# Kernel tuning notes

Hardware: AMD Instinct MI355X
Metric: run time of the kernel (lower is better)

## Reference

```python
import jax, jax.numpy as jnp
import numpy as np
from jax import lax

RATE = 2          # self.rate
KS = 3            # kernel_size for matching patches
FUSE_K = 3        # fuse_k
SCALE = 10.0      # softmax_scale
EPS = 1e-4        # NaN guard in l2 norm


def extract_patches(x, size=3, step=1):
    """ZeroPad2d(1) then unfold -> (B, L, C, size, size) with L = Ho*Wo."""
    B, C, H, W = x.shape
    p = lax.conv_general_dilated_patches(
        x, (size, size), (step, step), padding=((1, 1), (1, 1)))
    Ho, Wo = p.shape[2], p.shape[3]
    # feature dim ordering of patches is (C, kh, kw)
    p = p.reshape(B, C, size, size, Ho, Wo)
    return p.transpose(0, 4, 5, 1, 2, 3).reshape(B, Ho * Wo, C, size, size)


def fuse_conv(s):
    """Conv with identity eye(k) kernel, pad 1 (diagonal propagation)."""
    w = jnp.eye(FUSE_K, dtype=s.dtype).reshape(1, 1, FUSE_K, FUSE_K)
    return lax.conv_general_dilated(s, w, (1, 1), ((1, 1), (1, 1)))


def contextual_attention(foreground, background, mask):
    B, C, H, W = foreground.shape
    # raw patches used as deconv filters: (B, L, C, 2*rate, 2*rate)
    raw_w = extract_patches(background, size=2 * RATE, step=RATE)
    # nearest downsample by rate (F.interpolate nearest, scale 1/rate == stride slice)
    fg = foreground[:, :, ::RATE, ::RATE]
    bg = background[:, :, ::RATE, ::RATE]
    fh, fw = fg.shape[2], fg.shape[3]
    bh, bw = bg.shape[2], bg.shape[3]
    # matching patches: (B, L, C, 3, 3), L = bh*bw
    w = extract_patches(bg, KS, 1)
    # mask patches -> per-patch validity (code uses batch 0 of the mask only)
    m = mask[:, :, ::RATE, ::RATE]
    mp = extract_patches(m, KS, 1)[0]            # (L, 1, 3, 3)
    mm = jnp.mean(mp, axis=(1, 2, 3))            # (L,)
    eq = (mm == 0.0).astype(foreground.dtype)[None, :, None, None]  # (1, L, 1, 1)
    # cosine-normalized filters
    norm = jnp.sqrt(jnp.sum(w * w, axis=(2, 3, 4), keepdims=True))
    wn = w / jnp.maximum(norm, EPS)
    # per-batch dynamic conv: scores (B, L, fh, fw)
    def score(f, wi):
        return lax.conv_general_dilated(f[None], wi, (1, 1), ((1, 1), (1, 1)))[0]
    s = jax.vmap(score)(fg, wn)
    # fuse: two identity-kernel convs with raw reshapes (faithful to torch .view,
    # including the discarded second permute in the original code)
    s = s.reshape(B, 1, fh * fw, bh * bw)
    s = fuse_conv(s)
    s = s.reshape(B, fh, fw, bh, bw).transpose(0, 2, 1, 4, 3)
    s = s.reshape(B, 1, fh * fw, bh * bw)
    s = fuse_conv(s)
    s = s.reshape(B, bh * bw, fh, fw)  # raw row-major reinterpret, as torch .view does
    # masked scaled softmax over background-patch dim
    s = s * eq
    s = jax.nn.softmax(s * SCALE, axis=1) * eq
    # per-batch deconv with raw patches as filters (conv_transpose2d stride=rate, pad=1)
    def deconv(si, rwi):
        # torch conv_transpose2d(W:(L,C,4,4)) == dilated conv with flipped, swapped kernel
        wt = jnp.flip(rwi, axis=(-2, -1)).transpose(1, 0, 2, 3)  # (C, L, 4, 4)
        pad = 2 * RATE - 1 - 1  # k - 1 - padding = 2
        return lax.conv_general_dilated(
            si[None], wt, (1, 1), ((pad, pad), (pad, pad)),
            lhs_dilation=(RATE, RATE))[0]
    y = jax.vmap(deconv)(s, raw_w) / 4.0  # (B, C, H, W)
    return y


def setup_inputs() -> dict:
    key = jax.random.key(0)
    k1, k2, k3 = jax.random.split(key, 3)
    B, C, H, W = 8, 128, 64, 64
    foreground = jax.random.normal(k1, (B, C, H, W), jnp.float32)
    background = jax.random.normal(k2, (B, C, H, W), jnp.float32)
    mask = (jax.random.uniform(k3, (1, 1, H, W)) < 0.25).astype(jnp.float32)
    return {"foreground": foreground, "background": background, "mask": mask}


def reference(foreground, background, mask):
    return contextual_attention(foreground, background, mask)
```

## Files before the change

### kernel.cpp

```cpp
#include <hip/hip_runtime.h>

typedef _Float16 half8 __attribute__((ext_vector_type(8)));
typedef float f32x4 __attribute__((ext_vector_type(4)));
typedef unsigned short us8 __attribute__((ext_vector_type(8)));
typedef unsigned short ush;
typedef unsigned int uint32;

#define IMGB 295936u
#define WROW 8704u

#define OFF_FGH  0ull
#define OFF_BGH  2367488ull
#define OFF_BGL  4734976ull
#define OFF_BGT  7102464ull
#define OFF_SS   15523840ull
#define OFF_LIST 15589376ull
#define OFF_NACT 15593472ull
#define OFF_S0   15597568ull
#define OFF_S2   49152000ull
#define OFF_WGT2 82706432ull

static __device__ __forceinline__ ush f2h(float f) {
    union { _Float16 h; ush u; } c; c.h = (_Float16)f; return c.u;
}
static __device__ __forceinline__ float h2f(ush u) {
    union { _Float16 h; ush u; } c; c.u = u; return (float)c.h;
}
__device__ __forceinline__ int untr(int v) { return ((v & 31) << 5) | (v >> 5); }

__global__ void k_prep2(const float* __restrict__ fg, const float* __restrict__ bg,
                        const float* __restrict__ mask,
                        ush* __restrict__ fgh3, ush* __restrict__ bgh,
                        ush* __restrict__ bgl, ush* __restrict__ BGt,
                        float* __restrict__ SS, int* __restrict__ L,
                        int* __restrict__ nact) {
    int y = blockIdx.x, b = blockIdx.y, t = threadIdx.x;
    __shared__ float lds[64 * 129];
    __shared__ float fls[32 * 129];
    __shared__ float sm2[32][8];
    __shared__ int ps[256];
    if (y == 64) {
        if (b != 0) return;
        int fl[4], s = 0;
#pragma unroll
        for (int j = 0; j < 4; ++j) {
            int l = t * 4 + j;
            int hm = l >> 5, wm = l & 31;
            int any = 0;
            for (int di = -1; di <= 1; ++di)
                for (int dj = -1; dj <= 1; ++dj) {
                    int yy = hm + di, xxx = wm + dj;
                    if (yy >= 0 && yy < 32 && xxx >= 0 && xxx < 32)
                        any |= (mask[(2 * yy) * 64 + 2 * xxx] != 0.0f);
                }
            fl[j] = !any; s += fl[j];
        }
        ps[t] = s;
        __syncthreads();
        for (int off = 1; off < 256; off <<= 1) {
            int v = (t >= off) ? ps[t - off] : 0;
            __syncthreads();
            ps[t] += v;
            __syncthreads();
        }
        int base = ps[t] - s;
#pragma unroll
        for (int j = 0; j < 4; ++j)
            if (fl[j]) L[base++] = t * 4 + j;
        if (t == 255) nact[0] = ps[255];
        return;
    }
    int xx = t & 63;
    for (int c0 = 0; c0 < 128; c0 += 4) {
        int c = c0 + (t >> 6);
        lds[xx * 129 + c] = bg[((b * 128 + c) * 64 + y) * 64 + xx];
    }
    __syncthreads();
    uint32* dst = (uint32*)(BGt + (size_t)(b * 64 + y) * 8192);
    for (int j = t; j < 4096; j += 256) {
        int x = j >> 6, cp = (j & 63) * 2;
        uint32 h0 = f2h(lds[x * 129 + cp]);
        uint32 h1 = f2h(lds[x * 129 + cp + 1]);
        dst[j] = h0 | (h1 << 16);
    }
    if ((y & 1) != 0) return;
    int yd = y >> 1;
    {
        int xq = t & 31, cg = t >> 5;
        for (int c0 = 0; c0 < 128; c0 += 8) {
            int c = c0 + cg;
            fls[xq * 129 + c] = fg[((b * 128 + c) * 64 + y) * 64 + 2 * xq];
        }
    }
    {
        int xd = t & 31, part = t >> 5;
        float s = 0.f;
        int c0 = part * 16;
#pragma unroll
        for (int c = 0; c < 16; ++c) {
            float v = lds[(2 * xd) * 129 + c0 + c];
            s += v * v;
        }
        sm2[xd][part] = s;
    }
    __syncthreads();
    if (t < 32) {
        float s = 0.f;
#pragma unroll
        for (int p = 0; p < 8; ++p) s += sm2[t][p];
        SS[b * 1024 + yd * 32 + t] = s;
    }
    unsigned base = ((b * 34 + yd + 1) * 34 + 1) * 128;
    for (int k = t; k < 2048; k += 256) {
        int x = k >> 6, c = (k & 63) * 2;
        float vb0 = lds[(2 * x) * 129 + c], vb1 = lds[(2 * x) * 129 + c + 1];
        float vf0 = fls[x * 129 + c],       vf1 = fls[x * 129 + c + 1];
        _Float16 bh0 = (_Float16)vb0, bh1 = (_Float16)vb1;
        float br0 = vb0 - (float)bh0, br1 = vb1 - (float)bh1;
        union { _Float16 h; ush u; } x0, x1;
        x0.h = bh0; x1.h = bh1;
        uint32 b01 = (uint32)x0.u | ((uint32)x1.u << 16);
        uint32 l01 = (uint32)f2h(br0) | ((uint32)f2h(br1) << 16);
        ((uint32*)(bgh + base))[k] = b01;
        ((uint32*)(bgl + base))[k] = l01;
        uint32 f01 = (uint32)f2h(vf0) | ((uint32)f2h(vf1) << 16);
        int ch = c >> 6, g = (c >> 3) & 7, cl = c & 7;
        unsigned pix = (unsigned)(yd + 1) * 34 + (x + 1);
        unsigned ui = (((unsigned)(b * 16 + ch * 8 + g) * 1156 + pix) << 2) + (cl >> 1);
        ((uint32*)fgh3)[ui] = f01;
    }
    unsigned cb0 = ((unsigned)(b * 34 + yd + 1) * 34) * 64;
    if (t < 64) {
        ((uint32*)bgh)[cb0 + t] = 0; ((uint32*)bgl)[cb0 + t] = 0;
    } else if (t < 128) {
        unsigned cb1 = cb0 + 33 * 64 + (t - 64);
        ((uint32*)bgh)[cb1] = 0; ((uint32*)bgl)[cb1] = 0;
    } else if (t < 256) {
        int tt = t - 128;
        unsigned pix = (unsigned)(yd + 1) * 34 + ((tt >> 6) ? 33u : 0u);
        int pl = tt & 63, plane = pl >> 2, w = pl & 3;
        ((uint32*)fgh3)[(((unsigned)(b * 16 + plane) * 1156 + pix) << 2) + w] = 0;
    }
    if (yd == 0 || yd == 31) {
        int prow = (yd == 0) ? 0 : 33;
        unsigned rb = (unsigned)(b * 34 + prow) * 2176;
        for (int k = t; k < 2176; k += 256) {
            ((uint32*)bgh)[rb + k] = 0; ((uint32*)bgl)[rb + k] = 0;
            int plane = k / 136, rem = k - plane * 136;
            unsigned pix = (unsigned)prow * 34 + (rem >> 2);
            ((uint32*)fgh3)[(((unsigned)(b * 16 + plane) * 1156 + pix) << 2) + (rem & 3)] = 0;
        }
    }
}

__global__ __launch_bounds__(256, 2)
void k_smfma(const ush* __restrict__ fgh3, const ush* __restrict__ bgh,
             const ush* __restrict__ bgl, const float* __restrict__ SS,
             float* __restrict__ s0) {
    int qt = blockIdx.x, pt = blockIdx.y, b = blockIdx.z;
    int t = threadIdx.x, wid = t >> 6, lane = t & 63;
    int wp = wid >> 1, wq = wid & 1;
    __shared__ ulong2 smem_raw[3328];
    __shared__ float rnl[128];
    char* smem = (char*)smem_raw;

    if (t < 128) {
        int pr = (pt << 2) + (t >> 5), pc = t & 31;
        float n2 = 0.f;
#pragma unroll
        for (int di = -1; di <= 1; ++di) {
            int r = pr + di;
            if ((unsigned)r < 32u) {
                const float* Srow = SS + b * 1024 + r * 32;
#pragma unroll
                for (int dj = -1; dj <= 1; ++dj) {
                    int c2 = pc + dj;
                    if ((unsigned)c2 < 32u) n2 += Srow[c2];
                }
            }
        }
        rnl[t] = 1.0f / fmaxf(sqrtf(n2), 1e-4f);
    }

    const char* base0 = (const char*)bgh + (size_t)b * IMGB + (unsigned)(pt * 4) * WROW;
    const char* base1 = (const char*)bgl + (size_t)b * IMGB + (unsigned)(pt * 4) * WROW;

    f32x4 acc[4][4];
#pragma unroll
    for (int i = 0; i < 4; ++i)
#pragma unroll
        for (int j = 0; j < 4; ++j) acc[i][j] = (f32x4){0.f, 0.f, 0.f, 0.f};

    int r15 = lane & 15, hi2 = lane >> 4;
    for (int ch = 0; ch < 2; ++ch) {
        __syncthreads();
        {
            int pixl = (lane >> 3);
            int sl = lane & 7;
            for (int idx = wid; idx < 52; idx += 4) {
                int a = idx / 26;
                int chunk = idx - a * 26;
                int pix = chunk * 8 + pixl;
                int g = sl ^ (pix & 7);
                const char* sb = a ? base1 : base0;
                const char* gp = sb + ((unsigned)pix << 8) + ((unsigned)ch << 7)
                               + ((unsigned)g << 4);
                char* lp = smem + (unsigned)(a * 26624 + chunk * 1024);
                __builtin_amdgcn_global_load_lds(
                    (const __attribute__((address_space(1))) void*)gp,
                    (__attribute__((address_space(3))) void*)lp, 16, 0, 0);
            }
        }
        __syncthreads();

        const char* Aimg = (const char*)fgh3
                         + (((size_t)(b * 16 + ch * 8)) * 1156 + (unsigned)(qt * 136)) * 16;
        for (int o = 0; o < 9; ++o) {
            int dy = o / 3, dx = o - 3 * (o / 3);
            int pixB[4], pixA[4];
#pragma unroll
            for (int i = 0; i < 4; ++i) {
                pixB[i] = (wp * 2 + (i >> 1) + dy) * 34 + (i & 1) * 16 + r15 + dx;
                pixA[i] = (wq * 2 + (i >> 1) + dy) * 34 + (i & 1) * 16 + r15 + dx;
            }
#pragma unroll
            for (int cc = 0; cc < 2; ++cc) {
                int g = cc * 4 + hi2;
                half8 bh[4], bl[4], af[4];
#pragma unroll
                for (int i = 0; i < 4; ++i) {
                    unsigned offB = ((unsigned)pixB[i] << 7) + ((unsigned)(g ^ (pixB[i] & 7)) << 4);
                    bh[i] = *(const half8*)(smem + offB);
                    bl[i] = *(const half8*)(smem + 26624 + offB);
                    af[i] = *(const half8*)(Aimg + (((size_t)g * 1156 + pixA[i]) << 4));
                }
#pragma unroll
                for (int i = 0; i < 4; ++i)
#pragma unroll
                    for (int j = 0; j < 4; ++j) {
                        acc[i][j] = __builtin_amdgcn_mfma_f32_16x16x32_f16(bh[i], af[j], acc[i][j], 0, 0, 0);
                        acc[i][j] = __builtin_amdgcn_mfma_f32_16x16x32_f16(bl[i], af[j], acc[i][j], 0, 0, 0);
                    }
            }
        }
    }
    int col = lane & 15, rgrp = (lane >> 4) << 2;
#pragma unroll
    for (int i = 0; i < 4; ++i) {
        int Pl = wp * 64 + i * 16 + rgrp;
        int Pb = pt * 128 + Pl;
        float rn0 = rnl[Pl + 0];
        float rn1 = rnl[Pl + 1];
        float rn2 = rnl[Pl + 2];
        float rn3 = rnl[Pl + 3];
#pragma unroll
        for (int j = 0; j < 4; ++j) {
            int Q = qt * 128 + wq * 64 + j * 16 + col;
            float* dst = s0 + ((size_t)(b * 1024 + Pb) << 10) + Q;
            dst[0]    = acc[i][j][0] * rn0;
            dst[1024] = acc[i][j][1] * rn1;
            dst[2048] = acc[i][j][2] * rn2;
            dst[3072] = acc[i][j][3] * rn3;
        }
    }
}

__global__ void k_fuse(const float* __restrict__ s0, float* __restrict__ s2t,
                       const int* __restrict__ L, const int* __restrict__ nactp) {
    int nact = *nactp;
    int b = blockIdx.z;
    int u = blockIdx.x * 256 + threadIdx.x;
    int T = untr(u);
    const float* S = s0 + (size_t)b * 1048576;
    for (int ai = blockIdx.y; ai < nact; ai += 32) {
        int R = L[ai];
        float acc = 0.f;
#pragma unroll
        for (int k = -1; k <= 1; ++k) {
            int Rk = R + k, Tk = T + k;
            if ((unsigned)Rk < 1024u && (unsigned)Tk < 1024u) {
                int Pr = untr(Rk), Qc = untr(Tk);
#pragma unroll
                for (int j = -1; j <= 1; ++j) {
                    int r = Pr + j, cI = Qc + j;
                    if ((unsigned)r < 1024u && (unsigned)cI < 1024u)
                        acc += S[(size_t)r * 1024 + cI];
                }
            }
        }
        s2t[(size_t)b * 1048576 + (size_t)R * 1024 + u] = acc;
    }
}

__global__ __launch_bounds__(256)
void k_ctsw(const ush* __restrict__ BGt, const float* __restrict__ s2t,
            const int* __restrict__ L, const int* __restrict__ nactp,
            ush* __restrict__ CT, ush* __restrict__ W2) {
    int bx = blockIdx.x, b = blockIdx.y, t = threadIdx.x;
    int nact = *nactp;
    __shared__ float sm[32][8], sd[32][8];
    __shared__ float Msh[32], RDsh[32];
    __shared__ ush wt[32][136];
    if (bx < 16) {
        int KPAD = (nact + 31) & ~31;
        int ab = bx, a = ab >> 2, bb = ab & 3;
        for (int ai0 = 0; ai0 < KPAD; ai0 += 256) {
            int ai = ai0 + t;
            if (ai >= KPAD) break;
            int ok = 0;
            const ush* srow = nullptr;
            if (ai < nact) {
                int R = L[ai];
                int hb = R >> 5, wb = R & 31;
                int row = 2 * hb - 1 + a, col = 2 * wb - 1 + bb;
                if (row >= 0 && row < 64 && col >= 0 && col < 64) {
                    ok = 1;
                    srow = BGt + ((size_t)((b * 64 + row) * 64 + col) << 7);
                }
            }
            ush* dst = CT + ((size_t)(b * 16 + ab) << 15) + ai;
#pragma unroll 4
            for (int c = 0; c < 128; ++c)
                dst[(size_t)c << 8] = ok ? srow[c] : (ush)0;
        }
        return;
    }
    int uc = bx - 16;
    int u0 = uc * 32;
    int part = t >> 5, ul = t & 31;
    {
        const float* S = s2t + (size_t)b * 1048576 + u0 + ul;
        float m = -3e38f, d = 0.f;
        for (int ai = part; ai < nact; ai += 8) {
            float v = S[(size_t)L[ai] << 10];
            if (v > m) { d *= expf(10.f * (m - v)); m = v; }
            d += expf(10.f * (v - m));
        }
        sm[ul][part] = m; sd[ul][part] = d;
    }
    __syncthreads();
    if (t < 32) {
        float mm = -3e38f, dd = 0.f;
#pragma unroll
        for (int p = 0; p < 8; ++p) {
            float m2 = sm[t][p], d2 = sd[t][p];
            if (m2 > mm) { dd *= expf(10.f * (mm - m2)); mm = m2; dd += d2; }
            else dd += d2 * expf(10.f * (m2 - mm));
        }
        int cnt0 = 1024 - nact;
        if (cnt0 > 0) {
            if (mm < 0.f) { dd *= expf(10.f * mm); mm = 0.f; }
            dd += (float)cnt0 * expf(-10.f * mm);
        }
        Msh[t] = mm; RDsh[t] = 1.f / dd;
    }
    __syncthreads();
    for (int kp = 0; kp < 16; ++kp) {
        int k = kp * 8 + part;
        float w = 0.f;
        if (k < nact) {
            float v = s2t[((size_t)(b * 1024 + L[k]) << 10) + u0 + ul];
            w = expf(10.f * (v - Msh[ul])) * RDsh[ul];
        }
        wt[ul][k] = f2h(w);
    }
    __syncthreads();
    {
        int ur = t >> 3, kb = t & 7;
        int uu = u0 + ur;
        int p1 = (uu & 31) + 1, q1 = (uu >> 5) + 1;
        ush* dstr = W2 + (((size_t)(b * 35 + p1) * 35 + q1) << 7) + kb * 16;
        *(half8*)dstr       = *(const half8*)&wt[ur][kb * 16];
        *(half8*)(dstr + 8) = *(const half8*)&wt[ur][kb * 16 + 8];
    }
    for (int r = uc; r < 1225; r += 32) {
        int p1 = r / 35, q1 = r - p1 * 35;
        if (p1 < 1 || p1 > 32 || q1 < 1 || q1 > 32) {
            uint32* row = (uint32*)(W2 + (((size_t)(b * 35 + p1) * 35 + q1) << 7));
            if (t < 64) row[t] = 0;
        }
    }
}

__global__ __launch_bounds__(256, 4)
void k_dgemm(const ush* __restrict__ CT, const ush* __restrict__ W2,
             const int* __restrict__ nactp, float* __restrict__ y) {
    int nact = *nactp;
    int KPAD = (nact + 31) & ~31;
    int pt2 = blockIdx.x;
    int par = blockIdx.y, b = blockIdx.z;
    int a_lo = par >> 1, b_lo = par & 1;
    int P0 = 1 - a_lo, Q0 = 1 - b_lo;
    int p_lo = P0 + pt2;
    int wid = threadIdx.x >> 6, lane = threadIdx.x & 63;
    int r15 = lane & 15, kg = (lane >> 4) << 3;

    f32x4 acc[2][2];
#pragma unroll
    for (int i = 0; i < 2; ++i)
#pragma unroll
        for (int j = 0; j < 2; ++j) acc[i][j] = (f32x4){0.f, 0.f, 0.f, 0.f};

    for (int k0 = 0; k0 < KPAD; k0 += 32) {
#pragma unroll
        for (int pp = 0; pp < 2; ++pp)
#pragma unroll
            for (int qq = 0; qq < 2; ++qq) {
                int ab = (a_lo + 2 * pp) * 4 + (b_lo + 2 * qq);
                const ush* Ab = CT + ((size_t)(b * 16 + ab) << 15)
                              + ((unsigned)(wid * 32) << 8) + k0 + kg;
                int p1 = p_lo - pp + 1;
                int q1b = Q0 - qq + 1;
                const ush* Bb = W2 + (((size_t)(b * 35 + p1) * 35 + q1b) << 7) + k0 + kg;
                half8 A[2], B[2];
                A[0] = *(const half8*)(Ab + ((unsigned)r15 << 8));
                A[1] = *(const half8*)(Ab + ((unsigned)(16 + r15) << 8));
                B[0] = *(const half8*)(Bb + ((unsigned)r15 << 7));
                B[1] = *(const half8*)(Bb + ((unsigned)(16 + r15) << 7));
#pragma unroll
                for (int i = 0; i < 2; ++i)
#pragma unroll
                    for (int j = 0; j < 2; ++j)
                        acc[i][j] = __builtin_amdgcn_mfma_f32_16x16x32_f16(A[i], B[j], acc[i][j], 0, 0, 0);
            }
    }
    int col = r15, rgrp = (lane >> 4) << 2;
    int oy = 2 * p_lo + a_lo - 1;
#pragma unroll
    for (int i = 0; i < 2; ++i) {
        int c = wid * 32 + i * 16 + rgrp;
#pragma unroll
        for (int j = 0; j < 2; ++j) {
            int q_lo = Q0 + j * 16 + col;
            int ox = 2 * q_lo + b_lo - 1;
            float* Y = y + ((size_t)((b * 128 + c) * 64 + oy) << 6) + ox;
            Y[0]         = acc[i][j][0] * 0.25f;
            Y[4096]      = acc[i][j][1] * 0.25f;
            Y[2 * 4096]  = acc[i][j][2] * 0.25f;
            Y[3 * 4096]  = acc[i][j][3] * 0.25f;
        }
    }
}

extern "C" void kernel_launch(void* const* d_in, const int* in_sizes, int n_in,
                              void* d_out, int out_size, void* d_ws, size_t ws_size,
                              hipStream_t stream) {
    (void)in_sizes; (void)n_in; (void)out_size; (void)ws_size;
    const float* fg   = (const float*)d_in[0];
    const float* bg   = (const float*)d_in[1];
    const float* mask = (const float*)d_in[2];
    float* y = (float*)d_out;
    char* ws = (char*)d_ws;

    ush*   fgh3  = (ush*)(ws + OFF_FGH);
    ush*   bgh   = (ush*)(ws + OFF_BGH);
    ush*   bgl   = (ush*)(ws + OFF_BGL);
    ush*   BGt   = (ush*)(ws + OFF_BGT);
    float* SS    = (float*)(ws + OFF_SS);
    int*   Lst   = (int*)(ws + OFF_LIST);
    int*   nact  = (int*)(ws + OFF_NACT);
    float* s0    = (float*)(ws + OFF_S0);
    ush*   CT    = (ush*)(ws + OFF_S0);
    float* s2t   = (float*)(ws + OFF_S2);
    ush*   W2    = (ush*)(ws + OFF_WGT2);

    k_prep2<<<dim3(65, 8), 256, 0, stream>>>(fg, bg, mask, fgh3, bgh, bgl, BGt, SS, Lst, nact);
    k_smfma<<<dim3(8, 8, 8), 256, 0, stream>>>(fgh3, bgh, bgl, SS, s0);
    k_fuse<<<dim3(4, 32, 8), 256, 0, stream>>>(s0, s2t, Lst, nact);
    k_ctsw<<<dim3(48, 8), 256, 0, stream>>>(BGt, s2t, Lst, nact, CT, W2);
    k_dgemm<<<dim3(32, 4, 8), 256, 0, stream>>>(CT, W2, nact, y);
}
```

Before: 108.9 us.

## Stage fuse rows in shared memory and transpose CT via LDS tile

k_fuse now stages, for each active output row, the nine needed score rows into shared memory and computes all 1024 outputs of that row from LDS. This replaces scattered per-thread global gathers and avoids recomputing row indices. k_ctsw's CT build now loads 32 background rows with 16-byte vector loads into an LDS tile and writes the transpose as packed 32-bit words, instead of writing one ushort per thread with a 512-byte stride. Both changes add barriers and shared memory, and the fuse grid shrinks to 64x8 blocks.

```diff
diff --git a/kernel.cpp b/kernel.cpp
--- a/kernel.cpp
+++ b/kernel.cpp
@@ -265,30 +265,50 @@
     }
 }
 
-__global__ void k_fuse(const float* __restrict__ s0, float* __restrict__ s2t,
-                       const int* __restrict__ L, const int* __restrict__ nactp) {
+__global__ __launch_bounds__(256)
+void k_fuse(const float* __restrict__ s0, float* __restrict__ s2t,
+            const int* __restrict__ L, const int* __restrict__ nactp) {
     int nact = *nactp;
-    int b = blockIdx.z;
-    int u = blockIdx.x * 256 + threadIdx.x;
-    int T = untr(u);
+    int b = blockIdx.y, t = threadIdx.x;
+    __shared__ float rows9[9][1024];
     const float* S = s0 + (size_t)b * 1048576;
-    for (int ai = blockIdx.y; ai < nact; ai += 32) {
+    for (int ai = blockIdx.x; ai < nact; ai += 64) {
         int R = L[ai];
-        float acc = 0.f;
-#pragma unroll
-        for (int k = -1; k <= 1; ++k) {
-            int Rk = R + k, Tk = T + k;
-            if ((unsigned)Rk < 1024u && (unsigned)Tk < 1024u) {
-                int Pr = untr(Rk), Qc = untr(Tk);
-#pragma unroll
-                for (int j = -1; j <= 1; ++j) {
-                    int r = Pr + j, cI = Qc + j;
-                    if ((unsigned)r < 1024u && (unsigned)cI < 1024u)
-                        acc += S[(size_t)r * 1024 + cI];
+        __syncthreads();
+        for (int rr = 0; rr < 9; ++rr) {
+            int kk = rr / 3, jj = rr - kk * 3;
+            int Rk = R - 1 + kk;
+            int r = 0, valid = 0;
+            if ((unsigned)Rk < 1024u) {
+                r = untr(Rk) - 1 + jj;
+                valid = ((unsigned)r < 1024u);
+            }
+            const float* src = S + (size_t)(valid ? r : 0) * 1024;
+            for (int c = t; c < 1024; c += 256)
+                rows9[rr][c] = valid ? src[c] : 0.f;
+        }
+        __syncthreads();
+        float* dstR = s2t + (size_t)b * 1048576 + ((size_t)R << 10);
+#pragma unroll
+        for (int i = 0; i < 4; ++i) {
+            int v = t + i * 256;
+            int T = untr(v);
+            float acc = 0.f;
+#pragma unroll
+            for (int k = -1; k <= 1; ++k) {
+                int Tk = T + k;
+                if ((unsigned)Tk < 1024u) {
+                    int Qc = untr(Tk);
+#pragma unroll
+                    for (int j = -1; j <= 1; ++j) {
+                        int cI = Qc + j;
+                        if ((unsigned)cI < 1024u)
+                            acc += rows9[(k + 1) * 3 + (j + 1)][cI];
+                    }
                 }
             }
-        }
-        s2t[(size_t)b * 1048576 + (size_t)R * 1024 + u] = acc;
+            dstR[v] = acc;
+        }
     }
 }
 
@@ -301,27 +321,37 @@
     __shared__ float sm[32][8], sd[32][8];
     __shared__ float Msh[32], RDsh[32];
     __shared__ ush wt[32][136];
+    __shared__ ush tile[32][136];
     if (bx < 16) {
         int KPAD = (nact + 31) & ~31;
         int ab = bx, a = ab >> 2, bb = ab & 3;
-        for (int ai0 = 0; ai0 < KPAD; ai0 += 256) {
-            int ai = ai0 + t;
-            if (ai >= KPAD) break;
-            int ok = 0;
-            const ush* srow = nullptr;
-            if (ai < nact) {
-                int R = L[ai];
-                int hb = R >> 5, wb = R & 31;
-                int row = 2 * hb - 1 + a, col = 2 * wb - 1 + bb;
-                if (row >= 0 && row < 64 && col >= 0 && col < 64) {
-                    ok = 1;
-                    srow = BGt + ((size_t)((b * 64 + row) * 64 + col) << 7);
+        uint32* dstw = (uint32*)(CT + ((size_t)(b * 16 + ab) << 15));
+        for (int ai0 = 0; ai0 < KPAD; ai0 += 32) {
+            __syncthreads();
+            {
+                int ai = ai0 + (t >> 3), part = t & 7;
+                uint4 v0 = make_uint4(0, 0, 0, 0), v1 = make_uint4(0, 0, 0, 0);
+                if (ai < nact) {
+                    int R = L[ai];
+                    int hb = R >> 5, wb = R & 31;
+                    int row = 2 * hb - 1 + a, col = 2 * wb - 1 + bb;
+                    if (row >= 0 && row < 64 && col >= 0 && col < 64) {
+                        const ush* src = BGt + ((size_t)((b * 64 + row) * 64 + col) << 7);
+                        v0 = *(const uint4*)(src + part * 16);
+                        v1 = *(const uint4*)(src + part * 16 + 8);
+                    }
                 }
-            }
-            ush* dst = CT + ((size_t)(b * 16 + ab) << 15) + ai;
-#pragma unroll 4
-            for (int c = 0; c < 128; ++c)
-                dst[(size_t)c << 8] = ok ? srow[c] : (ush)0;
+                *(uint4*)&tile[t >> 3][part * 16] = v0;
+                *(uint4*)&tile[t >> 3][part * 16 + 8] = v1;
+            }
+            __syncthreads();
+            int aiw = t & 15, cb = t >> 4;
+#pragma unroll
+            for (int c2 = 0; c2 < 8; ++c2) {
+                int c = cb + c2 * 16;
+                uint32 w = (uint32)tile[aiw * 2][c] | ((uint32)tile[aiw * 2 + 1][c] << 16);
+                dstw[c * 128 + (ai0 >> 1) + aiw] = w;
+            }
         }
         return;
     }
@@ -466,7 +496,7 @@
 
     k_prep2<<<dim3(65, 8), 256, 0, stream>>>(fg, bg, mask, fgh3, bgh, bgl, BGt, SS, Lst, nact);
     k_smfma<<<dim3(8, 8, 8), 256, 0, stream>>>(fgh3, bgh, bgl, SS, s0);
-    k_fuse<<<dim3(4, 32, 8), 256, 0, stream>>>(s0, s2t, Lst, nact);
+    k_fuse<<<dim3(64, 8), 256, 0, stream>>>(s0, s2t, Lst, nact);
     k_ctsw<<<dim3(48, 8), 256, 0, stream>>>(BGt, s2t, Lst, nact, CT, W2);
     k_dgemm<<<dim3(32, 4, 8), 256, 0, stream>>>(CT, W2, nact, y);
 }
```

Result: slower. 115.8 us (+6.3%).

## Move background-patch transpose into score kernel grid and unroll offset loop

Applied to the files above, without the earlier changes.

The CT gather (transposing the background patches into the deconv operand layout) moves out of the softmax-weights kernel and runs as two extra z-slices of the MFMA score kernel. It now sits in its own workspace region, so it no longer aliases the s0 buffer. The aim is to overlap this memory-bound gather with the compute-bound score GEMM and to shorten the later kernel. The 9-offset loop in the score kernel is also fully unrolled, which may raise register pressure under the launch bound of 2 blocks per SM.

```diff
diff --git a/kernel.cpp b/kernel.cpp
--- a/kernel.cpp
+++ b/kernel.cpp
@@ -19,6 +19,7 @@
 #define OFF_S0   15597568ull
 #define OFF_S2   49152000ull
 #define OFF_WGT2 82706432ull
+#define OFF_CT   85215232ull
 
 static __device__ __forceinline__ ush f2h(float f) {
     union { _Float16 h; ush u; } c; c.h = (_Float16)f; return c.u;
@@ -156,9 +157,40 @@
 __global__ __launch_bounds__(256, 2)
 void k_smfma(const ush* __restrict__ fgh3, const ush* __restrict__ bgh,
              const ush* __restrict__ bgl, const float* __restrict__ SS,
+             const ush* __restrict__ BGt, const int* __restrict__ L,
+             const int* __restrict__ nactp, ush* __restrict__ CT,
              float* __restrict__ s0) {
-    int qt = blockIdx.x, pt = blockIdx.y, b = blockIdx.z;
-    int t = threadIdx.x, wid = t >> 6, lane = t & 63;
+    int qt = blockIdx.x, pt = blockIdx.y, z = blockIdx.z;
+    int t = threadIdx.x;
+    if (z >= 8) {
+        int nact = *nactp;
+        int KPAD = (nact + 31) & ~31;
+        int b2 = (z - 8) * 4 + (pt >> 1);
+        int ab = ((pt & 1) << 3) | qt;
+        int a = ab >> 2, bb = ab & 3;
+        for (int ai0 = 0; ai0 < KPAD; ai0 += 256) {
+            int ai = ai0 + t;
+            if (ai >= KPAD) break;
+            int ok = 0;
+            const ush* srow = nullptr;
+            if (ai < nact) {
+                int R = L[ai];
+                int hb = R >> 5, wb = R & 31;
+                int row = 2 * hb - 1 + a, col = 2 * wb - 1 + bb;
+                if (row >= 0 && row < 64 && col >= 0 && col < 64) {
+                    ok = 1;
+                    srow = BGt + ((size_t)((b2 * 64 + row) * 64 + col) << 7);
+                }
+            }
+            ush* dst = CT + ((size_t)(b2 * 16 + ab) << 15) + ai;
+#pragma unroll 4
+            for (int c = 0; c < 128; ++c)
+                dst[(size_t)c << 8] = ok ? srow[c] : (ush)0;
+        }
+        return;
+    }
+    int b = z;
+    int wid = t >> 6, lane = t & 63;
     int wp = wid >> 1, wq = wid & 1;
     __shared__ ulong2 smem_raw[3328];
     __shared__ float rnl[128];
@@ -215,6 +247,7 @@
 
         const char* Aimg = (const char*)fgh3
                          + (((size_t)(b * 16 + ch * 8)) * 1156 + (unsigned)(qt * 136)) * 16;
+#pragma unroll
         for (int o = 0; o < 9; ++o) {
             int dy = o / 3, dx = o - 3 * (o / 3);
             int pixB[4], pixA[4];
@@ -293,39 +326,13 @@
 }
 
 __global__ __launch_bounds__(256)
-void k_ctsw(const ush* __restrict__ BGt, const float* __restrict__ s2t,
-            const int* __restrict__ L, const int* __restrict__ nactp,
-            ush* __restrict__ CT, ush* __restrict__ W2) {
-    int bx = blockIdx.x, b = blockIdx.y, t = threadIdx.x;
+void k_ctsw(const float* __restrict__ s2t, const int* __restrict__ L,
+            const int* __restrict__ nactp, ush* __restrict__ W2) {
+    int uc = blockIdx.x, b = blockIdx.y, t = threadIdx.x;
     int nact = *nactp;
     __shared__ float sm[32][8], sd[32][8];
     __shared__ float Msh[32], RDsh[32];
     __shared__ ush wt[32][136];
-    if (bx < 16) {
-        int KPAD = (nact + 31) & ~31;
-        int ab = bx, a = ab >> 2, bb = ab & 3;
-        for (int ai0 = 0; ai0 < KPAD; ai0 += 256) {
-            int ai = ai0 + t;
-            if (ai >= KPAD) break;
-            int ok = 0;
-            const ush* srow = nullptr;
-            if (ai < nact) {
-                int R = L[ai];
-                int hb = R >> 5, wb = R & 31;
-                int row = 2 * hb - 1 + a, col = 2 * wb - 1 + bb;
-                if (row >= 0 && row < 64 && col >= 0 && col < 64) {
-                    ok = 1;
-                    srow = BGt + ((size_t)((b * 64 + row) * 64 + col) << 7);
-                }
-            }
-            ush* dst = CT + ((size_t)(b * 16 + ab) << 15) + ai;
-#pragma unroll 4
-            for (int c = 0; c < 128; ++c)
-                dst[(size_t)c << 8] = ok ? srow[c] : (ush)0;
-        }
-        return;
-    }
-    int uc = bx - 16;
     int u0 = uc * 32;
     int part = t >> 5, ul = t & 31;
     {
@@ -460,13 +467,13 @@
     int*   Lst   = (int*)(ws + OFF_LIST);
     int*   nact  = (int*)(ws + OFF_NACT);
     float* s0    = (float*)(ws + OFF_S0);
-    ush*   CT    = (ush*)(ws + OFF_S0);
     float* s2t   = (float*)(ws + OFF_S2);
     ush*   W2    = (ush*)(ws + OFF_WGT2);
+    ush*   CT    = (ush*)(ws + OFF_CT);
 
     k_prep2<<<dim3(65, 8), 256, 0, stream>>>(fg, bg, mask, fgh3, bgh, bgl, BGt, SS, Lst, nact);
-    k_smfma<<<dim3(8, 8, 8), 256, 0, stream>>>(fgh3, bgh, bgl, SS, s0);
+    k_smfma<<<dim3(8, 8, 10), 256, 0, stream>>>(fgh3, bgh, bgl, SS, BGt, Lst, nact, CT, s0);
     k_fuse<<<dim3(4, 32, 8), 256, 0, stream>>>(s0, s2t, Lst, nact);
-    k_ctsw<<<dim3(48, 8), 256, 0, stream>>>(BGt, s2t, Lst, nact, CT, W2);
+    k_ctsw<<<dim3(32, 8), 256, 0, stream>>>(s2t, Lst, nact, W2);
     k_dgemm<<<dim3(32, 4, 8), 256, 0, stream>>>(CT, W2, nact, y);
 }
```

Measured after the change: 152.6 us. +40.2%, slower.
